# Kernel optimization log

Measured on AMD Instinct MI355X. Metric: run time of the kernel, lower is better.

## Reference

```python
import jax, jax.numpy as jnp
import numpy as np

HIDDEN = 4096
N_HEADS = 32
N_KV_HEADS = 8
HEAD_DIM = HIDDEN // N_HEADS  # 128
KV_DIM = N_KV_HEADS * HEAD_DIM  # 1024
ROPE_THETA = 10000.0
B, S = 1, 2048


def setup_inputs() -> dict:
    key = jax.random.key(0)
    ks = jax.random.split(key, 5)
    scale = 0.02
    return {
        "positions": jnp.arange(B * S, dtype=jnp.int32).reshape(B, S),
        "hidden_states": jax.random.normal(ks[0], (B, S, HIDDEN), dtype=jnp.float32),
        "Wqkv": jax.random.normal(ks[1], (HIDDEN, HIDDEN + 2 * KV_DIM), dtype=jnp.float32) * scale,
        "bqkv": jax.random.normal(ks[2], (HIDDEN + 2 * KV_DIM,), dtype=jnp.float32) * scale,
        "Wproj": jax.random.normal(ks[3], (HIDDEN, HIDDEN), dtype=jnp.float32) * scale,
        "bproj": jax.random.normal(ks[4], (HIDDEN,), dtype=jnp.float32) * scale,
    }


def _apply_rope(x, positions):
    # x: [B, S, H, D]; NeoX-style rotation over full head_dim (vLLM get_rope default)
    half = HEAD_DIM // 2
    inv_freq = 1.0 / (ROPE_THETA ** (jnp.arange(0, half, dtype=jnp.float32) / half))
    angles = positions.astype(jnp.float32)[..., None] * inv_freq  # [B, S, half]
    cos = jnp.cos(angles)[:, :, None, :]  # [B, S, 1, half]
    sin = jnp.sin(angles)[:, :, None, :]
    x1, x2 = x[..., :half], x[..., half:]
    return jnp.concatenate([x1 * cos - x2 * sin, x2 * cos + x1 * sin], axis=-1)


def reference(positions, hidden_states, Wqkv, bqkv, Wproj, bproj):
    b, s, _ = hidden_states.shape
    qkv = hidden_states @ Wqkv + bqkv  # [B, S, HIDDEN + 2*KV_DIM]
    q, k, v = jnp.split(qkv, [HIDDEN, HIDDEN + KV_DIM], axis=-1)
    q = q.reshape(b, s, N_HEADS, HEAD_DIM)
    k = k.reshape(b, s, N_KV_HEADS, HEAD_DIM)
    v = v.reshape(b, s, N_KV_HEADS, HEAD_DIM)

    q = _apply_rope(q, positions)
    k = _apply_rope(k, positions)

    # GQA: expand kv heads to query heads (4 query heads per kv head)
    rep = N_HEADS // N_KV_HEADS
    k = jnp.repeat(k, rep, axis=2)  # [B, S, N_HEADS, D]
    v = jnp.repeat(v, rep, axis=2)

    scaling = 1.0 / np.sqrt(HEAD_DIM).astype(np.float32)
    scores = jnp.einsum("bqhd,bkhd->bhqk", q, k) * scaling  # [B, H, S, S]
    causal = jnp.tril(jnp.ones((s, s), dtype=bool))
    scores = jnp.where(causal[None, None], scores, jnp.finfo(scores.dtype).min)
    probs = jax.nn.softmax(scores, axis=-1)
    attn = jnp.einsum("bhqk,bkhd->bqhd", probs, v).reshape(b, s, HIDDEN)

    return attn @ Wproj + bproj
```

## Files before the change

kernel.cpp:

```cpp
#include <hip/hip_runtime.h>

#define HIDDEN 4096
#define NHEADS 32
#define NKV 8
#define HD 128
#define KVD 1024
#define QKVN 6144
#define SEQ 2048

typedef unsigned short u16;
typedef __bf16 bf16x8 __attribute__((ext_vector_type(8)));
typedef float f32x4 __attribute__((ext_vector_type(4)));

__device__ __forceinline__ u16 f2b(float f) {
  union { float f; unsigned u; } v; v.f = f;
  unsigned r = (v.u + 0x7fffu + ((v.u >> 16) & 1u)) >> 16;
  return (u16)r;
}

__device__ __forceinline__ void gl_lds16(const void* g, void* l) {
  __builtin_amdgcn_global_load_lds(
      (const __attribute__((address_space(1))) unsigned*)g,
      (__attribute__((address_space(3))) unsigned*)l, 16, 0, 0);
}

__device__ __forceinline__ f32x4 mfma16(bf16x8 a, bf16x8 b, f32x4 c) {
  return __builtin_amdgcn_mfma_f32_16x16x32_bf16(a, b, c, 0, 0, 0);
}

__global__ void cvt_bf16(const float* __restrict__ x, u16* __restrict__ y, int n) {
  int i = (blockIdx.x * 256 + threadIdx.x) * 4;
  if (i < n) {
    float4 v = *(const float4*)(x + i);
    u16* o = y + i;
    o[0] = f2b(v.x); o[1] = f2b(v.y); o[2] = f2b(v.z); o[3] = f2b(v.w);
  }
}

__global__ void transpose_cvt(const float* __restrict__ W, long ldW,
                              u16* __restrict__ Wt, long ldT) {
  __shared__ float tile[32][33];
  long c0 = blockIdx.x * 32L, r0 = blockIdx.y * 32L;
  int tx = threadIdx.x, ty = threadIdx.y;
#pragma unroll
  for (int i = 0; i < 32; i += 8)
    tile[ty + i][tx] = W[(r0 + ty + i) * ldW + c0 + tx];
  __syncthreads();
#pragma unroll
  for (int i = 0; i < 32; i += 8)
    Wt[(c0 + ty + i) * ldT + r0 + tx] = f2b(tile[tx][ty + i]);
}

__global__ __launch_bounds__(256) void gemm_bt_bias(
    const u16* __restrict__ A, const u16* __restrict__ Bt,
    const float* __restrict__ bias, float* __restrict__ C,
    int M, int N, int K) {
  __shared__ u16 As[128 * 32];
  __shared__ u16 Bs[128 * 32];
  const int t = threadIdx.x;
  const int w = t >> 6, lane = t & 63, quad = lane >> 4, l15 = lane & 15;
  const int wy = w >> 1, wx = w & 1;
  const long m0 = blockIdx.y * 128L, n0 = blockIdx.x * 128L;
  f32x4 acc[4][4] = {};
  const u16* Ag = A + (m0 + (t >> 2)) * (long)K + (t & 3) * 8;
  const u16* Bg = Bt + (n0 + (t >> 2)) * (long)K + (t & 3) * 8;
  char* lA0 = (char*)As + w * 1024;
  char* lA1 = (char*)As + 4096 + w * 1024;
  char* lB0 = (char*)Bs + w * 1024;
  char* lB1 = (char*)Bs + 4096 + w * 1024;
  const long k64 = 64L * K;
  for (int k0 = 0; k0 < K; k0 += 32) {
    gl_lds16(Ag + k0, lA0);
    gl_lds16(Ag + k64 + k0, lA1);
    gl_lds16(Bg + k0, lB0);
    gl_lds16(Bg + k64 + k0, lB1);
    __syncthreads();
    bf16x8 af[4], bfr[4];
#pragma unroll
    for (int mi = 0; mi < 4; ++mi)
      af[mi] = *reinterpret_cast<const bf16x8*>(&As[(wy * 64 + mi * 16 + l15) * 32 + quad * 8]);
#pragma unroll
    for (int nj = 0; nj < 4; ++nj)
      bfr[nj] = *reinterpret_cast<const bf16x8*>(&Bs[(wx * 64 + nj * 16 + l15) * 32 + quad * 8]);
#pragma unroll
    for (int mi = 0; mi < 4; ++mi)
#pragma unroll
      for (int nj = 0; nj < 4; ++nj)
        acc[mi][nj] = mfma16(af[mi], bfr[nj], acc[mi][nj]);
    __syncthreads();
  }
#pragma unroll
  for (int mi = 0; mi < 4; ++mi) {
#pragma unroll
    for (int nj = 0; nj < 4; ++nj) {
      long n = n0 + wx * 64 + nj * 16 + l15;
      float bv = bias[n];
      long mrow = m0 + wy * 64 + mi * 16 + quad * 4;
#pragma unroll
      for (int r = 0; r < 4; ++r)
        C[(mrow + r) * (long)N + n] = acc[mi][nj][r] + bv;
    }
  }
}

__global__ void rope_qk(const float* __restrict__ qkv, const int* __restrict__ pos,
                        u16* __restrict__ Qr, u16* __restrict__ Kr) {
  int s = blockIdx.x;
  int hl = threadIdx.x >> 6;
  int d = threadIdx.x & 63;
  int h = blockIdx.y * 4 + hl;
  float p = (float)pos[s];
  float inv = __builtin_amdgcn_exp2f(-(float)d * (13.287712379549449f / 64.0f));
  float ang = p * inv;
  float cs, sn;
  __sincosf(ang, &sn, &cs);
  long base = (long)s * QKVN + (long)h * HD;
  float x1 = qkv[base + d], x2 = qkv[base + d + 64];
  float o1 = x1 * cs - x2 * sn, o2 = x2 * cs + x1 * sn;
  if (h < NHEADS) {
    const float sc = 0.12751744154f;
    long ob = ((long)h * SEQ + s) * HD;
    Qr[ob + d] = f2b(o1 * sc);
    Qr[ob + d + 64] = f2b(o2 * sc);
  } else {
    long ob = ((long)(h - NHEADS) * SEQ + s) * HD;
    Kr[ob + d] = f2b(o1);
    Kr[ob + d + 64] = f2b(o2);
  }
}

__device__ __forceinline__ void attn_tile(
    const bf16x8 q[4], const u16* KsF, const u16* VsF, u16* Psw,
    bool diag, int wq, int quad, int l15, f32x4 Oa[8], f32x4& lacc,
    bf16x8 ones) {
  f32x4 s[4] = {};
#pragma unroll
  for (int ks = 0; ks < 4; ++ks) {
#pragma unroll
    for (int nj = 0; nj < 4; ++nj) {
      bf16x8 bk = *reinterpret_cast<const bf16x8*>(
          &KsF[ks * 2048 + (nj * 16 + l15) * 32 + quad * 8]);
      s[nj] = mfma16(q[ks], bk, s[nj]);
    }
  }
#pragma unroll
  for (int nj = 0; nj < 4; ++nj) {
    int key = nj * 16 + l15;
    int ksw = key >> 5, kc = key & 31;
#pragma unroll
    for (int r = 0; r < 4; ++r) {
      float x = s[nj][r];
      if (diag && key > wq + r) x = -3.0e30f;
      Psw[ksw * 512 + (quad * 4 + r) * 32 + kc] = f2b(__builtin_amdgcn_exp2f(x));
    }
  }
#pragma unroll
  for (int ks = 0; ks < 2; ++ks) {
    bf16x8 ap = *reinterpret_cast<const bf16x8*>(&Psw[ks * 512 + l15 * 32 + quad * 8]);
    lacc = mfma16(ap, ones, lacc);
#pragma unroll
    for (int dj = 0; dj < 8; ++dj) {
      bf16x8 bv = *reinterpret_cast<const bf16x8*>(
          &VsF[ks * 4096 + (dj * 16 + l15) * 32 + quad * 8]);
      Oa[dj] = mfma16(ap, bv, Oa[dj]);
    }
  }
}

__global__ __launch_bounds__(256) void attn_fused(
    const u16* __restrict__ Qr, const u16* __restrict__ Kr,
    const u16* __restrict__ Vt, u16* __restrict__ Ao) {
  __shared__ u16 Ks[4 * 64 * 32];
  __shared__ u16 Vs[2 * 128 * 32];
  __shared__ u16 Ps[4][2 * 16 * 32];
  const int px = blockIdx.x, h = blockIdx.y, kvh = h >> 2;
  const int qtA = px, qtB = (SEQ / 64 - 1) - px;
  const int t = threadIdx.x, w = t >> 6, lane = t & 63;
  const int quad = lane >> 4, l15 = lane & 15;
  const int wq = w * 16 + quad * 4;
  u16* Psw = &Ps[w][0];

  bf16x8 ones;
  {
    union { u16 u[8]; bf16x8 v; } ou;
#pragma unroll
    for (int i = 0; i < 8; ++i) ou.u[i] = 0x3F80;
    ones = ou.v;
  }

  bf16x8 qA[4], qB[4];
  {
    const u16* QgA = Qr + ((long)h * SEQ + qtA * 64) * HD;
    const u16* QgB = Qr + ((long)h * SEQ + qtB * 64) * HD;
    long go = (long)(w * 16 + (lane >> 2)) * HD + (lane & 3) * 8;
#pragma unroll
    for (int j = 0; j < 4; ++j) {
      gl_lds16(QgA + go + j * 32, (char*)Ks + j * 4096 + w * 1024);
      gl_lds16(QgB + go + j * 32, (char*)Vs + j * 4096 + w * 1024);
    }
    __syncthreads();
#pragma unroll
    for (int j = 0; j < 4; ++j) {
      qA[j] = *reinterpret_cast<const bf16x8*>(&Ks[j * 2048 + (w * 16 + l15) * 32 + quad * 8]);
      qB[j] = *reinterpret_cast<const bf16x8*>(&Vs[j * 2048 + (w * 16 + l15) * 32 + quad * 8]);
    }
    __syncthreads();
  }

  f32x4 OaA[8] = {}, OaB[8] = {};
  f32x4 lA = {}, lB = {};
  const u16* Kg0 = Kr + (long)kvh * SEQ * HD;
  const u16* Vg0 = Vt + (long)kvh * HD * SEQ;

  for (int kt = 0; kt <= qtB; ++kt) {
    const int k0 = kt * 64;
    {
      const u16* Kg = Kg0 + (long)k0 * HD;
      long go = (long)(w * 16 + (lane >> 2)) * HD + (lane & 3) * 8;
#pragma unroll
      for (int j = 0; j < 4; ++j)
        gl_lds16(Kg + go + j * 32, (char*)Ks + j * 4096 + w * 1024);
      const u16* Vg = Vg0 + k0;
#pragma unroll
      for (int j = 0; j < 4; ++j) {
        int off = j * 2048 + w * 512 + lane * 8;
        int ks = off >> 12, rem = off & 4095;
        int dd = rem >> 5, kc = rem & 31;
        gl_lds16(Vg + (long)dd * SEQ + ks * 32 + kc, (char*)Vs + j * 4096 + w * 1024);
      }
    }
    __syncthreads();

    attn_tile(qB, Ks, Vs, Psw, kt == qtB, wq, quad, l15, OaB, lB, ones);
    if (kt <= qtA)
      attn_tile(qA, Ks, Vs, Psw, kt == qtA, wq, quad, l15, OaA, lA, ones);

    __syncthreads();
  }

#pragma unroll
  for (int r = 0; r < 4; ++r) {
    float invA = 1.0f / lA[r];
    float invB = 1.0f / lB[r];
    long rowA = (long)(qtA * 64 + w * 16 + quad * 4 + r) * HIDDEN + (long)h * HD;
    long rowB = (long)(qtB * 64 + w * 16 + quad * 4 + r) * HIDDEN + (long)h * HD;
#pragma unroll
    for (int dj = 0; dj < 8; ++dj) {
      Ao[rowA + dj * 16 + l15] = f2b(OaA[dj][r] * invA);
      Ao[rowB + dj * 16 + l15] = f2b(OaB[dj][r] * invB);
    }
  }
}

extern "C" void kernel_launch(void* const* d_in, const int* in_sizes, int n_in,
                              void* d_out, int out_size, void* d_ws, size_t ws_size,
                              hipStream_t stream) {
  const int* positions = (const int*)d_in[0];
  const float* hidden = (const float*)d_in[1];
  const float* Wqkv = (const float*)d_in[2];
  const float* bqkv = (const float*)d_in[3];
  const float* Wproj = (const float*)d_in[4];
  const float* bproj = (const float*)d_in[5];
  float* out = (float*)d_out;
  char* ws = (char*)d_ws;

  u16* Wqt = (u16*)(ws);
  u16* Wpt = (u16*)(ws + 50331648L);
  u16* Xb = (u16*)(ws + 83886080L);
  float* QKV = (float*)(ws + 100663296L);
  u16* Qr = (u16*)(ws + 150994944L);
  u16* Kr = (u16*)(ws + 167772160L);
  u16* Vt = (u16*)(ws + 171966464L);
  u16* Ao = (u16*)(ws + 176160768L);

  cvt_bf16<<<8192, 256, 0, stream>>>(hidden, Xb, SEQ * HIDDEN);
  transpose_cvt<<<dim3(QKVN / 32, HIDDEN / 32), dim3(32, 8), 0, stream>>>(Wqkv, QKVN, Wqt, HIDDEN);
  transpose_cvt<<<dim3(HIDDEN / 32, HIDDEN / 32), dim3(32, 8), 0, stream>>>(Wproj, HIDDEN, Wpt, HIDDEN);
  gemm_bt_bias<<<dim3(QKVN / 128, SEQ / 128), 256, 0, stream>>>(Xb, Wqt, bqkv, QKV, SEQ, QKVN, HIDDEN);
  rope_qk<<<dim3(SEQ, 10), 256, 0, stream>>>(QKV, positions, Qr, Kr);
  transpose_cvt<<<dim3(KVD / 32, SEQ / 32), dim3(32, 8), 0, stream>>>(QKV + 5120, QKVN, Vt, SEQ);
  attn_fused<<<dim3(SEQ / 128, NHEADS), 256, 0, stream>>>(Qr, Kr, Vt, Ao);
  gemm_bt_bias<<<dim3(HIDDEN / 128, SEQ / 128), 256, 0, stream>>>(Ao, Wpt, bproj, out, SEQ, HIDDEN, HIDDEN);
}
```

Before: 597.3 us.

## Fuse RoPE, scaling and V transpose into QKV GEMM epilogue

Adds a dedicated QKV GEMM whose epilogue applies bias, RoPE and Q scaling per head tile and writes bf16 Q/K plus a transposed V directly. This drops the fp32 QKV intermediate and two extra kernels. The wave layout changes to 32x128 per wave so each wave holds both halves of a head. The weight-transpose and input-convert kernels also switch to 64x64 tiles with vectorized loads and stores. The risks are higher register pressure from 16 accumulators per wave and strided Vt stores.

```diff
diff --git a/kernel.cpp b/kernel.cpp
--- a/kernel.cpp
+++ b/kernel.cpp
@@ -11,6 +11,7 @@
 typedef unsigned short u16;
 typedef __bf16 bf16x8 __attribute__((ext_vector_type(8)));
 typedef float f32x4 __attribute__((ext_vector_type(4)));
+typedef unsigned short u16x4 __attribute__((ext_vector_type(4)));
 
 __device__ __forceinline__ u16 f2b(float f) {
   union { float f; unsigned u; } v; v.f = f;
@@ -32,23 +33,32 @@
   int i = (blockIdx.x * 256 + threadIdx.x) * 4;
   if (i < n) {
     float4 v = *(const float4*)(x + i);
-    u16* o = y + i;
-    o[0] = f2b(v.x); o[1] = f2b(v.y); o[2] = f2b(v.z); o[3] = f2b(v.w);
-  }
-}
-
-__global__ void transpose_cvt(const float* __restrict__ W, long ldW,
-                              u16* __restrict__ Wt, long ldT) {
-  __shared__ float tile[32][33];
-  long c0 = blockIdx.x * 32L, r0 = blockIdx.y * 32L;
+    u16x4 o = {f2b(v.x), f2b(v.y), f2b(v.z), f2b(v.w)};
+    *(u16x4*)(y + i) = o;
+  }
+}
+
+__global__ void transpose_cvt64(const float* __restrict__ W, long ldW,
+                                u16* __restrict__ Wt, long ldT) {
+  __shared__ float tile[64][65];
+  long c0 = blockIdx.x * 64L, r0 = blockIdx.y * 64L;
   int tx = threadIdx.x, ty = threadIdx.y;
 #pragma unroll
-  for (int i = 0; i < 32; i += 8)
-    tile[ty + i][tx] = W[(r0 + ty + i) * ldW + c0 + tx];
+  for (int i = 0; i < 4; ++i) {
+    float4 v = *(const float4*)(W + (r0 + ty + i * 16) * ldW + c0 + tx * 4);
+    tile[ty + i * 16][tx * 4 + 0] = v.x;
+    tile[ty + i * 16][tx * 4 + 1] = v.y;
+    tile[ty + i * 16][tx * 4 + 2] = v.z;
+    tile[ty + i * 16][tx * 4 + 3] = v.w;
+  }
   __syncthreads();
 #pragma unroll
-  for (int i = 0; i < 32; i += 8)
-    Wt[(c0 + ty + i) * ldT + r0 + tx] = f2b(tile[tx][ty + i]);
+  for (int i = 0; i < 4; ++i) {
+    int c = ty + i * 16;
+    u16x4 o = {f2b(tile[tx * 4 + 0][c]), f2b(tile[tx * 4 + 1][c]),
+               f2b(tile[tx * 4 + 2][c]), f2b(tile[tx * 4 + 3][c])};
+    *(u16x4*)(Wt + (c0 + c) * ldT + r0 + tx * 4) = o;
+  }
 }
 
 __global__ __launch_bounds__(256) void gemm_bt_bias(
@@ -103,29 +113,97 @@
   }
 }
 
-__global__ void rope_qk(const float* __restrict__ qkv, const int* __restrict__ pos,
-                        u16* __restrict__ Qr, u16* __restrict__ Kr) {
-  int s = blockIdx.x;
-  int hl = threadIdx.x >> 6;
-  int d = threadIdx.x & 63;
-  int h = blockIdx.y * 4 + hl;
-  float p = (float)pos[s];
-  float inv = __builtin_amdgcn_exp2f(-(float)d * (13.287712379549449f / 64.0f));
-  float ang = p * inv;
-  float cs, sn;
-  __sincosf(ang, &sn, &cs);
-  long base = (long)s * QKVN + (long)h * HD;
-  float x1 = qkv[base + d], x2 = qkv[base + d + 64];
-  float o1 = x1 * cs - x2 * sn, o2 = x2 * cs + x1 * sn;
-  if (h < NHEADS) {
-    const float sc = 0.12751744154f;
-    long ob = ((long)h * SEQ + s) * HD;
-    Qr[ob + d] = f2b(o1 * sc);
-    Qr[ob + d + 64] = f2b(o2 * sc);
+__global__ __launch_bounds__(256) void gemm_qkv(
+    const u16* __restrict__ A, const u16* __restrict__ Bt,
+    const float* __restrict__ bias, const int* __restrict__ pos,
+    u16* __restrict__ Qr, u16* __restrict__ Kr, u16* __restrict__ Vt) {
+  __shared__ u16 As[128 * 32];
+  __shared__ u16 Bs[128 * 32];
+  const int K = HIDDEN;
+  const int t = threadIdx.x;
+  const int w = t >> 6, lane = t & 63, quad = lane >> 4, l15 = lane & 15;
+  const long m0 = blockIdx.y * 128L, n0 = blockIdx.x * 128L;
+  f32x4 acc[2][8] = {};
+  const u16* Ag = A + (m0 + (t >> 2)) * (long)K + (t & 3) * 8;
+  const u16* Bg = Bt + (n0 + (t >> 2)) * (long)K + (t & 3) * 8;
+  char* lA0 = (char*)As + w * 1024;
+  char* lA1 = (char*)As + 4096 + w * 1024;
+  char* lB0 = (char*)Bs + w * 1024;
+  char* lB1 = (char*)Bs + 4096 + w * 1024;
+  const long k64 = 64L * K;
+  for (int k0 = 0; k0 < K; k0 += 32) {
+    gl_lds16(Ag + k0, lA0);
+    gl_lds16(Ag + k64 + k0, lA1);
+    gl_lds16(Bg + k0, lB0);
+    gl_lds16(Bg + k64 + k0, lB1);
+    __syncthreads();
+    bf16x8 af[2], bfr[8];
+#pragma unroll
+    for (int mi = 0; mi < 2; ++mi)
+      af[mi] = *reinterpret_cast<const bf16x8*>(&As[(w * 32 + mi * 16 + l15) * 32 + quad * 8]);
+#pragma unroll
+    for (int nj = 0; nj < 8; ++nj)
+      bfr[nj] = *reinterpret_cast<const bf16x8*>(&Bs[(nj * 16 + l15) * 32 + quad * 8]);
+#pragma unroll
+    for (int mi = 0; mi < 2; ++mi)
+#pragma unroll
+      for (int nj = 0; nj < 8; ++nj)
+        acc[mi][nj] = mfma16(af[mi], bfr[nj], acc[mi][nj]);
+    __syncthreads();
+  }
+
+  const int tile = (int)(n0 >> 7);
+  float bv[8];
+#pragma unroll
+  for (int nj = 0; nj < 8; ++nj) bv[nj] = bias[n0 + nj * 16 + l15];
+
+  if (tile < 40) {
+    const bool isQ = tile < 32;
+    const float scq = 0.12751744154f;
+    u16* outp = isQ ? (Qr + (long)tile * SEQ * HD)
+                    : (Kr + (long)(tile - 32) * SEQ * HD);
+    float invf[4];
+#pragma unroll
+    for (int nj = 0; nj < 4; ++nj) {
+      float d = (float)(nj * 16 + l15);
+      invf[nj] = __builtin_amdgcn_exp2f(-d * (13.287712379549449f / 64.0f));
+    }
+#pragma unroll
+    for (int mi = 0; mi < 2; ++mi) {
+#pragma unroll
+      for (int r = 0; r < 4; ++r) {
+        long s = m0 + w * 32 + mi * 16 + quad * 4 + r;
+        float p = (float)pos[s];
+        u16* rowp = outp + s * HD;
+#pragma unroll
+        for (int nj = 0; nj < 4; ++nj) {
+          float ang = p * invf[nj];
+          float cs, sn;
+          __sincosf(ang, &sn, &cs);
+          float x1 = acc[mi][nj][r] + bv[nj];
+          float x2 = acc[mi][nj + 4][r] + bv[nj + 4];
+          float o1 = x1 * cs - x2 * sn;
+          float o2 = x2 * cs + x1 * sn;
+          if (isQ) { o1 *= scq; o2 *= scq; }
+          rowp[nj * 16 + l15] = f2b(o1);
+          rowp[nj * 16 + l15 + 64] = f2b(o2);
+        }
+      }
+    }
   } else {
-    long ob = ((long)(h - NHEADS) * SEQ + s) * HD;
-    Kr[ob + d] = f2b(o1);
-    Kr[ob + d + 64] = f2b(o2);
+    const int kvh = tile - 40;
+    u16* outp = Vt + (long)kvh * HD * SEQ;
+#pragma unroll
+    for (int mi = 0; mi < 2; ++mi) {
+      long s_base = m0 + w * 32 + mi * 16 + quad * 4;
+#pragma unroll
+      for (int nj = 0; nj < 8; ++nj) {
+        int d = nj * 16 + l15;
+        u16x4 o = {f2b(acc[mi][nj][0] + bv[nj]), f2b(acc[mi][nj][1] + bv[nj]),
+                   f2b(acc[mi][nj][2] + bv[nj]), f2b(acc[mi][nj][3] + bv[nj])};
+        *(u16x4*)(outp + (long)d * SEQ + s_base) = o;
+      }
+    }
   }
 }
 
@@ -267,18 +345,15 @@
   u16* Wqt = (u16*)(ws);
   u16* Wpt = (u16*)(ws + 50331648L);
   u16* Xb = (u16*)(ws + 83886080L);
-  float* QKV = (float*)(ws + 100663296L);
-  u16* Qr = (u16*)(ws + 150994944L);
-  u16* Kr = (u16*)(ws + 167772160L);
-  u16* Vt = (u16*)(ws + 171966464L);
-  u16* Ao = (u16*)(ws + 176160768L);
+  u16* Qr = (u16*)(ws + 100663296L);
+  u16* Kr = (u16*)(ws + 117440512L);
+  u16* Vt = (u16*)(ws + 121634816L);
+  u16* Ao = (u16*)(ws + 125829120L);
 
   cvt_bf16<<<8192, 256, 0, stream>>>(hidden, Xb, SEQ * HIDDEN);
-  transpose_cvt<<<dim3(QKVN / 32, HIDDEN / 32), dim3(32, 8), 0, stream>>>(Wqkv, QKVN, Wqt, HIDDEN);
-  transpose_cvt<<<dim3(HIDDEN / 32, HIDDEN / 32), dim3(32, 8), 0, stream>>>(Wproj, HIDDEN, Wpt, HIDDEN);
-  gemm_bt_bias<<<dim3(QKVN / 128, SEQ / 128), 256, 0, stream>>>(Xb, Wqt, bqkv, QKV, SEQ, QKVN, HIDDEN);
-  rope_qk<<<dim3(SEQ, 10), 256, 0, stream>>>(QKV, positions, Qr, Kr);
-  transpose_cvt<<<dim3(KVD / 32, SEQ / 32), dim3(32, 8), 0, stream>>>(QKV + 5120, QKVN, Vt, SEQ);
+  transpose_cvt64<<<dim3(QKVN / 64, HIDDEN / 64), dim3(16, 16), 0, stream>>>(Wqkv, QKVN, Wqt, HIDDEN);
+  transpose_cvt64<<<dim3(HIDDEN / 64, HIDDEN / 64), dim3(16, 16), 0, stream>>>(Wproj, HIDDEN, Wpt, HIDDEN);
+  gemm_qkv<<<dim3(QKVN / 128, SEQ / 128), 256, 0, stream>>>(Xb, Wqt, bqkv, positions, Qr, Kr, Vt);
   attn_fused<<<dim3(SEQ / 128, NHEADS), 256, 0, stream>>>(Qr, Kr, Vt, Ao);
   gemm_bt_bias<<<dim3(HIDDEN / 128, SEQ / 128), 256, 0, stream>>>(Ao, Wpt, bproj, out, SEQ, HIDDEN, HIDDEN);
 }
```

Result: slower. 632.2 us (+5.8%).
